# Performance work log

Measured on AMD Instinct MI355X. Metric: run time of the kernel, lower is better.

Reference implementation:

```python
import jax, jax.numpy as jnp
import numpy as np

SE_TEMP = 0.2
BN_EPS = 1e-5

def _l2n(x):
    # F.normalize(p=2, dim=-1) with eps=1e-12 clamp on the norm
    n = jnp.linalg.norm(x, axis=-1, keepdims=True)
    return x / jnp.maximum(n, 1e-12)

def setup_inputs() -> dict:
    key = jax.random.key(0)
    k1, k2, k3, k4, k5 = jax.random.split(key, 5)
    Q, I, D = 256, 2048, 256
    return {
        "query_feats": jax.random.normal(k1, (Q, D), dtype=jnp.float32),
        "query_img_feats": jax.random.normal(k2, (Q, D), dtype=jnp.float32),
        "gallery_img_feats": jax.random.normal(k3, (I, D), dtype=jnp.float32),
        "bn_gamma": jnp.ones((D,), dtype=jnp.float32),
        "bn_beta": jnp.zeros((D,), dtype=jnp.float32),
        "bn_mean": jax.random.normal(k4, (D,), dtype=jnp.float32) * 0.1,
        "bn_var": jax.random.uniform(k5, (D,), dtype=jnp.float32, minval=0.5, maxval=1.5),
    }

def reference(query_feats, query_img_feats, gallery_img_feats, bn_gamma, bn_beta, bn_mean, bn_var):
    # GalleryFilterNetwork.get_scores, mode='combined', gfn_activation_mode='se'
    inv_std = bn_gamma / jnp.sqrt(bn_var + BN_EPS)

    def bn(x):  # eval-mode BatchNorm1d over last dim D
        return (x - bn_mean) * inv_std + bn_beta

    xq = _l2n(query_feats)        # [Q, D] normalized query box feats
    yq = _l2n(query_img_feats)    # [Q, D] normalized query scene feats
    yg = _l2n(gallery_img_feats)  # [I, D] normalized gallery scene feats

    gate = jax.nn.sigmoid(xq / SE_TEMP)           # [Q, D]
    fused_query = bn(yq * gate)                   # [Q, D]  (non-p SE fuse)
    fused_gal = bn(yg[:, None, :] * gate[None])   # [I, Q, D] (p=True SE fuse)

    # cosine similarity per (q, i) pair, then sigmoid
    scores = jax.nn.sigmoid(
        jnp.einsum('qd,iqd->qi', _l2n(fused_query), _l2n(fused_gal))
    )
    return scores  # [Q, I]
```

## Files before the change

### kernel.cpp

```cpp
#include <hip/hip_runtime.h>
#include <math.h>

#define D 256
#define Q 256
#define I 2048

__device__ __forceinline__ float wave_sum(float v) {
#pragma unroll
    for (int off = 1; off < 64; off <<= 1)
        v += __shfl_xor(v, off, 64);
    return v;
}

__device__ __forceinline__ float sigmoidf_(float x) {
    return 1.0f / (1.0f + expf(-x));
}

__global__ void __launch_bounds__(256)
prep_all(const float* __restrict__ qf,
         const float* __restrict__ qif,
         const float* __restrict__ gal,
         const float* __restrict__ gamma,
         const float* __restrict__ beta,
         const float* __restrict__ mean,
         const float* __restrict__ var,
         float* __restrict__ p,
         float* __restrict__ w,
         float* __restrict__ v2,
         float* __restrict__ ygT,
         float* __restrict__ sq,
         float* __restrict__ ccp) {
    const int t = threadIdx.x;
    const int wv = t >> 6;
    const int l  = t & 63;

    if (blockIdx.x < 64) {
        __shared__ float tile[32][257];
        __shared__ float sinv[32];
        const int i0 = blockIdx.x * 32;
        const float4* g4 = (const float4*)gal;

#pragma unroll
        for (int c = 0; c < 8; c++) {
            int row = c * 4 + wv;
            float4 r = g4[(size_t)(i0 + row) * 64 + l];
            *(float4*)&tile[row][4 * l] = r;
        }
        __syncthreads();

#pragma unroll
        for (int k = 0; k < 8; k++) {
            int row = k * 4 + wv;
            float4 v = *(const float4*)&tile[row][4 * l];
            float s = wave_sum(v.x * v.x + v.y * v.y + v.z * v.z + v.w * v.w);
            if (l == 0) sinv[row] = 1.0f / fmaxf(sqrtf(s), 1e-12f);
        }
        __syncthreads();

        const int half = l >> 5, col = l & 31;
        const float si = sinv[col];
#pragma unroll
        for (int c = 0; c < 32; c++) {
            int d = c * 8 + wv * 2 + half;
            ygT[(size_t)d * I + i0 + col] = tile[col][d] * si;
        }
    } else {
        const int q = (blockIdx.x - 64) * 4 + wv;
        const float4* qf4  = (const float4*)qf;
        const float4* qif4 = (const float4*)qif;
        const float4* ga4  = (const float4*)gamma;
        const float4* be4  = (const float4*)beta;
        const float4* me4  = (const float4*)mean;
        const float4* va4  = (const float4*)var;

        float4 x = qf4[(size_t)q * 64 + l];
        float nx = wave_sum(x.x * x.x + x.y * x.y + x.z * x.z + x.w * x.w);
        float inx = 1.0f / fmaxf(sqrtf(nx), 1e-12f);
        float g0 = sigmoidf_(x.x * inx * 5.0f);
        float g1 = sigmoidf_(x.y * inx * 5.0f);
        float g2 = sigmoidf_(x.z * inx * 5.0f);
        float g3 = sigmoidf_(x.w * inx * 5.0f);

        float4 y = qif4[(size_t)q * 64 + l];
        float ny = wave_sum(y.x * y.x + y.y * y.y + y.z * y.z + y.w * y.w);
        float iny = 1.0f / fmaxf(sqrtf(ny), 1e-12f);

        float4 gm = ga4[l], bt = be4[l], mn = me4[l], vr = va4[l];
        float is0 = gm.x * rsqrtf(vr.x + 1e-5f);
        float is1 = gm.y * rsqrtf(vr.y + 1e-5f);
        float is2 = gm.z * rsqrtf(vr.z + 1e-5f);
        float is3 = gm.w * rsqrtf(vr.w + 1e-5f);
        float c0 = bt.x - mn.x * is0;
        float c1 = bt.y - mn.y * is1;
        float c2 = bt.z - mn.z * is2;
        float c3 = bt.w - mn.w * is3;
        float a0 = g0 * is0, a1 = g1 * is1, a2 = g2 * is2, a3 = g3 * is3;

        float f0 = y.x * iny * a0 + c0;
        float f1 = y.y * iny * a1 + c1;
        float f2 = y.z * iny * a2 + c2;
        float f3 = y.w * iny * a3 + c3;
        float nf = wave_sum(f0 * f0 + f1 * f1 + f2 * f2 + f3 * f3);
        float inf_ = 1.0f / fmaxf(sqrtf(nf), 1e-12f);
        float u0 = f0 * inf_, u1 = f1 * inf_, u2 = f2 * inf_, u3 = f3 * inf_;

        float4 pw = make_float4(u0 * a0, u1 * a1, u2 * a2, u3 * a3);
        float4 ww = make_float4(a0 * a0, a1 * a1, a2 * a2, a3 * a3);
        float4 vv = make_float4(2.0f * a0 * c0, 2.0f * a1 * c1,
                                2.0f * a2 * c2, 2.0f * a3 * c3);
        ((float4*)p)[(size_t)q * 64 + l]  = pw;
        ((float4*)w)[(size_t)q * 64 + l]  = ww;
        ((float4*)v2)[(size_t)q * 64 + l] = vv;

        float s = wave_sum(u0 * c0 + u1 * c1 + u2 * c2 + u3 * c3);
        if (l == 0) sq[q] = s;

        if (q == 0) {
            float ccs = wave_sum(c0 * c0 + c1 * c1 + c2 * c2 + c3 * c3);
            if (l == 0) *ccp = ccs;
        }
    }
}

#define ACC_STEP(yv, P_, W_, V_)                 \
    {                                            \
        a1.x += (P_) * yv.x;                     \
        a1.y += (P_) * yv.y;                     \
        a1.z += (P_) * yv.z;                     \
        a1.w += (P_) * yv.w;                     \
        float t0 = (W_) * yv.x + (V_);           \
        float t1 = (W_) * yv.y + (V_);           \
        float t2 = (W_) * yv.z + (V_);           \
        float t3 = (W_) * yv.w + (V_);           \
        a2.x += yv.x * t0;                       \
        a2.y += yv.y * t1;                       \
        a2.z += yv.z * t2;                       \
        a2.w += yv.w * t3;                       \
    }

__global__ void __launch_bounds__(256)
main_scores(const float* __restrict__ ygT,
            const float* __restrict__ p,
            const float* __restrict__ w,
            const float* __restrict__ v2,
            const float* __restrict__ sq,
            const float* __restrict__ ccp,
            float* __restrict__ out) {
    const int t = threadIdx.x, wv = t >> 6, lane = t & 63;
    const int q = __builtin_amdgcn_readfirstlane(blockIdx.x * 4 + wv);
    const float4* __restrict__ P = (const float4*)(p + (size_t)q * D);
    const float4* __restrict__ W = (const float4*)(w + (size_t)q * D);
    const float4* __restrict__ V = (const float4*)(v2 + (size_t)q * D);
    const float4* __restrict__ Yg = (const float4*)ygT;
    const int icol = blockIdx.y * 64 + lane;

    float4 a1 = make_float4(0.f, 0.f, 0.f, 0.f);
    float4 a2 = make_float4(0.f, 0.f, 0.f, 0.f);

#pragma unroll 2
    for (int dc = 0; dc < 64; ++dc) {
        float4 pp = P[dc], ww = W[dc], vv = V[dc];
        const float4* yb = Yg + (size_t)(dc * 4) * (I / 4) + icol;
        float4 y0 = yb[0 * (I / 4)];
        float4 y1 = yb[1 * (I / 4)];
        float4 y2 = yb[2 * (I / 4)];
        float4 y3 = yb[3 * (I / 4)];
        ACC_STEP(y0, pp.x, ww.x, vv.x);
        ACC_STEP(y1, pp.y, ww.y, vv.y);
        ACC_STEP(y2, pp.z, ww.z, vv.z);
        ACC_STEP(y3, pp.w, ww.w, vv.w);
    }

    const float s = sq[q];
    const float cc = *ccp;
    float4 o;
    o.x = sigmoidf_((a1.x + s) / fmaxf(sqrtf(fmaxf(a2.x + cc, 0.f)), 1e-12f));
    o.y = sigmoidf_((a1.y + s) / fmaxf(sqrtf(fmaxf(a2.y + cc, 0.f)), 1e-12f));
    o.z = sigmoidf_((a1.z + s) / fmaxf(sqrtf(fmaxf(a2.z + cc, 0.f)), 1e-12f));
    o.w = sigmoidf_((a1.w + s) / fmaxf(sqrtf(fmaxf(a2.w + cc, 0.f)), 1e-12f));
    ((float4*)out)[(size_t)q * (I / 4) + icol] = o;
}

extern "C" void kernel_launch(void* const* d_in, const int* in_sizes, int n_in,
                              void* d_out, int out_size, void* d_ws, size_t ws_size,
                              hipStream_t stream) {
    const float* qf    = (const float*)d_in[0];
    const float* qif   = (const float*)d_in[1];
    const float* gal   = (const float*)d_in[2];
    const float* gamma = (const float*)d_in[3];
    const float* beta  = (const float*)d_in[4];
    const float* mean  = (const float*)d_in[5];
    const float* var   = (const float*)d_in[6];
    float* out = (float*)d_out;

    float* ws  = (float*)d_ws;
    float* p   = ws;
    float* w   = p  + Q * D;
    float* v2  = w  + Q * D;
    float* ygT = v2 + Q * D;
    float* sq  = ygT + (size_t)D * I;
    float* cc  = sq + Q;

    prep_all<<<128, 256, 0, stream>>>(qf, qif, gal, gamma, beta, mean, var,
                                      p, w, v2, ygT, sq, cc);
    main_scores<<<dim3(Q / 4, I / 256), 256, 0, stream>>>(ygT, p, w, v2, sq, cc, out);
}
```

Before: 90.21 us.

## Retile main scoring kernel to two queries by two gallery columns per thread

Each wave now handles two queries and each lane two gallery columns loaded as float2, replacing one query by four columns. Every loaded gallery value is reused across two queries, halving gallery traffic per output, and each thread carries the same number of accumulators. The trade-off is narrower float2 loads, scalar per-element loads of the p/w/v2 vectors (the old code used float4), and a grid of 32x16 = 512 blocks, the same count as before.

```diff
diff --git a/kernel.cpp b/kernel.cpp
--- a/kernel.cpp
+++ b/kernel.cpp
@@ -122,22 +122,6 @@
     }
 }
 
-#define ACC_STEP(yv, P_, W_, V_)                 \
-    {                                            \
-        a1.x += (P_) * yv.x;                     \
-        a1.y += (P_) * yv.y;                     \
-        a1.z += (P_) * yv.z;                     \
-        a1.w += (P_) * yv.w;                     \
-        float t0 = (W_) * yv.x + (V_);           \
-        float t1 = (W_) * yv.y + (V_);           \
-        float t2 = (W_) * yv.z + (V_);           \
-        float t3 = (W_) * yv.w + (V_);           \
-        a2.x += yv.x * t0;                       \
-        a2.y += yv.y * t1;                       \
-        a2.z += yv.z * t2;                       \
-        a2.w += yv.w * t3;                       \
-    }
-
 __global__ void __launch_bounds__(256)
 main_scores(const float* __restrict__ ygT,
             const float* __restrict__ p,
@@ -147,38 +131,46 @@
             const float* __restrict__ ccp,
             float* __restrict__ out) {
     const int t = threadIdx.x, wv = t >> 6, lane = t & 63;
-    const int q = __builtin_amdgcn_readfirstlane(blockIdx.x * 4 + wv);
-    const float4* __restrict__ P = (const float4*)(p + (size_t)q * D);
-    const float4* __restrict__ W = (const float4*)(w + (size_t)q * D);
-    const float4* __restrict__ V = (const float4*)(v2 + (size_t)q * D);
-    const float4* __restrict__ Yg = (const float4*)ygT;
-    const int icol = blockIdx.y * 64 + lane;
+    const int qa = __builtin_amdgcn_readfirstlane(blockIdx.x * 8 + wv * 2);
+    const int qb = qa + 1;
+    const int ib = blockIdx.y * 128 + lane * 2;
 
-    float4 a1 = make_float4(0.f, 0.f, 0.f, 0.f);
-    float4 a2 = make_float4(0.f, 0.f, 0.f, 0.f);
+    const float* __restrict__ Pa = p  + (size_t)qa * D;
+    const float* __restrict__ Wa = w  + (size_t)qa * D;
+    const float* __restrict__ Va = v2 + (size_t)qa * D;
+    const float* __restrict__ Pb = p  + (size_t)qb * D;
+    const float* __restrict__ Wb = w  + (size_t)qb * D;
+    const float* __restrict__ Vb = v2 + (size_t)qb * D;
 
-#pragma unroll 2
-    for (int dc = 0; dc < 64; ++dc) {
-        float4 pp = P[dc], ww = W[dc], vv = V[dc];
-        const float4* yb = Yg + (size_t)(dc * 4) * (I / 4) + icol;
-        float4 y0 = yb[0 * (I / 4)];
-        float4 y1 = yb[1 * (I / 4)];
-        float4 y2 = yb[2 * (I / 4)];
-        float4 y3 = yb[3 * (I / 4)];
-        ACC_STEP(y0, pp.x, ww.x, vv.x);
-        ACC_STEP(y1, pp.y, ww.y, vv.y);
-        ACC_STEP(y2, pp.z, ww.z, vv.z);
-        ACC_STEP(y3, pp.w, ww.w, vv.w);
+    float2 a1a = make_float2(0.f, 0.f), a2a = make_float2(0.f, 0.f);
+    float2 a1b = make_float2(0.f, 0.f), a2b = make_float2(0.f, 0.f);
+
+#pragma unroll 8
+    for (int d = 0; d < D; ++d) {
+        float2 y = *(const float2*)&ygT[(size_t)d * I + ib];
+        float pa = Pa[d], wa = Wa[d], va = Va[d];
+        float pb = Pb[d], wb = Wb[d], vb = Vb[d];
+
+        a1a.x += pa * y.x;  a1a.y += pa * y.y;
+        float ta0 = wa * y.x + va;
+        float ta1 = wa * y.y + va;
+        a2a.x += y.x * ta0; a2a.y += y.y * ta1;
+
+        a1b.x += pb * y.x;  a1b.y += pb * y.y;
+        float tb0 = wb * y.x + vb;
+        float tb1 = wb * y.y + vb;
+        a2b.x += y.x * tb0; a2b.y += y.y * tb1;
     }
 
-    const float s = sq[q];
     const float cc = *ccp;
-    float4 o;
-    o.x = sigmoidf_((a1.x + s) / fmaxf(sqrtf(fmaxf(a2.x + cc, 0.f)), 1e-12f));
-    o.y = sigmoidf_((a1.y + s) / fmaxf(sqrtf(fmaxf(a2.y + cc, 0.f)), 1e-12f));
-    o.z = sigmoidf_((a1.z + s) / fmaxf(sqrtf(fmaxf(a2.z + cc, 0.f)), 1e-12f));
-    o.w = sigmoidf_((a1.w + s) / fmaxf(sqrtf(fmaxf(a2.w + cc, 0.f)), 1e-12f));
-    ((float4*)out)[(size_t)q * (I / 4) + icol] = o;
+    const float sa = sq[qa], sb = sq[qb];
+    float2 oa, ob;
+    oa.x = sigmoidf_((a1a.x + sa) / fmaxf(sqrtf(fmaxf(a2a.x + cc, 0.f)), 1e-12f));
+    oa.y = sigmoidf_((a1a.y + sa) / fmaxf(sqrtf(fmaxf(a2a.y + cc, 0.f)), 1e-12f));
+    ob.x = sigmoidf_((a1b.x + sb) / fmaxf(sqrtf(fmaxf(a2b.x + cc, 0.f)), 1e-12f));
+    ob.y = sigmoidf_((a1b.y + sb) / fmaxf(sqrtf(fmaxf(a2b.y + cc, 0.f)), 1e-12f));
+    *(float2*)&out[(size_t)qa * I + ib] = oa;
+    *(float2*)&out[(size_t)qb * I + ib] = ob;
 }
 
 extern "C" void kernel_launch(void* const* d_in, const int* in_sizes, int n_in,
@@ -203,5 +195,5 @@
 
     prep_all<<<128, 256, 0, stream>>>(qf, qif, gal, gamma, beta, mean, var,
                                       p, w, v2, ygT, sq, cc);
-    main_scores<<<dim3(Q / 4, I / 256), 256, 0, stream>>>(ygT, p, w, v2, sq, cc, out);
+    main_scores<<<dim3(Q / 8, I / 128), 256, 0, stream>>>(ygT, p, w, v2, sq, cc, out);
 }
```

Measured after the change: 94.71 us. 5.0% more time.

## Block gallery transpose into 256-column panels and register-prefetch Y loads

Applied to the files above, without the earlier changes.

The normalized gallery matrix is now stored as 8 contiguous panels of D x 256, one per blockIdx.y, so each main-kernel block streams a compact 256 KB region instead of strided rows of the full I-wide transpose. The main loop also adds a two-deep register double buffer that loads the next Y float4 values ahead of the FMA work, to hide global-load latency. The cost is more live registers, which may lower occupancy.

```diff
diff --git a/kernel.cpp b/kernel.cpp
--- a/kernel.cpp
+++ b/kernel.cpp
@@ -27,7 +27,7 @@
          float* __restrict__ p,
          float* __restrict__ w,
          float* __restrict__ v2,
-         float* __restrict__ ygT,
+         float* __restrict__ Y3,
          float* __restrict__ sq,
          float* __restrict__ ccp) {
     const int t = threadIdx.x;
@@ -57,12 +57,15 @@
         }
         __syncthreads();
 
+        const int iblk = i0 >> 8;
+        const int ioff = i0 & 255;
         const int half = l >> 5, col = l & 31;
         const float si = sinv[col];
+        float* dst = Y3 + (size_t)iblk * (D * 256) + ioff + col;
 #pragma unroll
         for (int c = 0; c < 32; c++) {
             int d = c * 8 + wv * 2 + half;
-            ygT[(size_t)d * I + i0 + col] = tile[col][d] * si;
+            dst[(size_t)d * 256] = tile[col][d] * si;
         }
     } else {
         const int q = (blockIdx.x - 64) * 4 + wv;
@@ -139,7 +142,7 @@
     }
 
 __global__ void __launch_bounds__(256)
-main_scores(const float* __restrict__ ygT,
+main_scores(const float* __restrict__ Y3,
             const float* __restrict__ p,
             const float* __restrict__ w,
             const float* __restrict__ v2,
@@ -148,27 +151,39 @@
             float* __restrict__ out) {
     const int t = threadIdx.x, wv = t >> 6, lane = t & 63;
     const int q = __builtin_amdgcn_readfirstlane(blockIdx.x * 4 + wv);
-    const float4* __restrict__ P = (const float4*)(p + (size_t)q * D);
-    const float4* __restrict__ W = (const float4*)(w + (size_t)q * D);
+    const float4* __restrict__ P = (const float4*)(p  + (size_t)q * D);
+    const float4* __restrict__ W = (const float4*)(w  + (size_t)q * D);
     const float4* __restrict__ V = (const float4*)(v2 + (size_t)q * D);
-    const float4* __restrict__ Yg = (const float4*)ygT;
-    const int icol = blockIdx.y * 64 + lane;
+    const float* __restrict__ Yb =
+        Y3 + (size_t)blockIdx.y * (D * 256) + lane * 4;
 
     float4 a1 = make_float4(0.f, 0.f, 0.f, 0.f);
     float4 a2 = make_float4(0.f, 0.f, 0.f, 0.f);
 
+    float4 buf[2][4];
+#pragma unroll
+    for (int c = 0; c < 2; c++)
+#pragma unroll
+        for (int j = 0; j < 4; j++)
+            buf[c][j] = *(const float4*)&Yb[(size_t)(c * 4 + j) * 256];
+
 #pragma unroll 2
     for (int dc = 0; dc < 64; ++dc) {
+        float4 cur0 = buf[dc & 1][0];
+        float4 cur1 = buf[dc & 1][1];
+        float4 cur2 = buf[dc & 1][2];
+        float4 cur3 = buf[dc & 1][3];
+        if (dc + 2 < 64) {
+#pragma unroll
+            for (int j = 0; j < 4; j++)
+                buf[dc & 1][j] =
+                    *(const float4*)&Yb[(size_t)((dc + 2) * 4 + j) * 256];
+        }
         float4 pp = P[dc], ww = W[dc], vv = V[dc];
-        const float4* yb = Yg + (size_t)(dc * 4) * (I / 4) + icol;
-        float4 y0 = yb[0 * (I / 4)];
-        float4 y1 = yb[1 * (I / 4)];
-        float4 y2 = yb[2 * (I / 4)];
-        float4 y3 = yb[3 * (I / 4)];
-        ACC_STEP(y0, pp.x, ww.x, vv.x);
-        ACC_STEP(y1, pp.y, ww.y, vv.y);
-        ACC_STEP(y2, pp.z, ww.z, vv.z);
-        ACC_STEP(y3, pp.w, ww.w, vv.w);
+        ACC_STEP(cur0, pp.x, ww.x, vv.x);
+        ACC_STEP(cur1, pp.y, ww.y, vv.y);
+        ACC_STEP(cur2, pp.z, ww.z, vv.z);
+        ACC_STEP(cur3, pp.w, ww.w, vv.w);
     }
 
     const float s = sq[q];
@@ -178,7 +193,7 @@
     o.y = sigmoidf_((a1.y + s) / fmaxf(sqrtf(fmaxf(a2.y + cc, 0.f)), 1e-12f));
     o.z = sigmoidf_((a1.z + s) / fmaxf(sqrtf(fmaxf(a2.z + cc, 0.f)), 1e-12f));
     o.w = sigmoidf_((a1.w + s) / fmaxf(sqrtf(fmaxf(a2.w + cc, 0.f)), 1e-12f));
-    ((float4*)out)[(size_t)q * (I / 4) + icol] = o;
+    *(float4*)&out[(size_t)q * I + blockIdx.y * 256 + lane * 4] = o;
 }
 
 extern "C" void kernel_launch(void* const* d_in, const int* in_sizes, int n_in,
@@ -197,11 +212,11 @@
     float* p   = ws;
     float* w   = p  + Q * D;
     float* v2  = w  + Q * D;
-    float* ygT = v2 + Q * D;
-    float* sq  = ygT + (size_t)D * I;
+    float* Y3  = v2 + Q * D;
+    float* sq  = Y3 + (size_t)D * I;
     float* cc  = sq + Q;
 
     prep_all<<<128, 256, 0, stream>>>(qf, qif, gal, gamma, beta, mean, var,
-                                      p, w, v2, ygT, sq, cc);
-    main_scores<<<dim3(Q / 4, I / 256), 256, 0, stream>>>(ygT, p, w, v2, sq, cc, out);
-}
+                                      p, w, v2, Y3, sq, cc);
+    main_scores<<<dim3(Q / 4, I / 256), 256, 0, stream>>>(Y3, p, w, v2, sq, cc, out);
+}
```

Measured after the change: 97.27 us. 1.08x slower.
